# Performance work log

Measured on AMD Instinct MI355X. Metric: run time of the kernel, lower is better.

The kernel has to match this reference:

```python
import jax, jax.numpy as jnp
import numpy as np

SEQ, BATCH, IN_DIM, HID = 2048, 64, 512, 512


def setup_inputs() -> dict:
    key = jax.random.key(0)
    ks = jax.random.split(key, 9)
    cat = IN_DIM + HID
    s = 1.0 / np.sqrt(cat)  # torch Linear default init scale
    inputs = jax.random.normal(ks[0], (SEQ, BATCH, IN_DIM), dtype=jnp.float32)
    def lin(k):
        kw, kb = jax.random.split(k)
        W = jax.random.uniform(kw, (cat, HID), jnp.float32, -s, s)
        b = jax.random.uniform(kb, (HID,), jnp.float32, -s, s)
        return W, b
    Wf, bf = lin(ks[1])
    Wi, bi = lin(ks[2])
    Wg, bg = lin(ks[3])
    Wo, bo = lin(ks[4])
    return {"inputs": inputs, "Wf": Wf, "bf": bf, "Wi": Wi, "bi": bi,
            "Wg": Wg, "bg": bg, "Wo": Wo, "bo": bo}


def reference(inputs, Wf, bf, Wi, bi, Wg, bg, Wo, bo):
    # inputs: (seq, batch, in_dim). Weights stored as (in+hid, hid) so
    # combined @ W + b matches torch's Linear on concat([x, hx]).
    batch = inputs.shape[1]
    hx0 = jnp.zeros((batch, HID), inputs.dtype)
    cx0 = jnp.zeros((batch, HID), inputs.dtype)

    def step(carry, x):
        hx, cx = carry
        combined = jnp.concatenate([x, hx], axis=1)  # (batch, in+hid)
        f = jax.nn.sigmoid(combined @ Wf + bf)
        i = jax.nn.sigmoid(combined @ Wi + bi)
        g = jnp.tanh(combined @ Wg + bg)
        o = jax.nn.sigmoid(combined @ Wo + bo)
        cx = f * cx + i * g
        hx = o * jnp.tanh(cx)
        return (hx, cx), hx

    (hx, cx), outputs = jax.lax.scan(step, (hx0, cx0), inputs)
    return outputs, (hx, cx)
```

## Files before the change

### kernel.cpp

```cpp
#include <hip/hip_runtime.h>
#include <hip/hip_bf16.h>


#define SEQ 2048
#define NBATCH 64
#define IN_DIM 512
#define HID 512
#define NB 64
#define GB 16

typedef __bf16 bf16x8 __attribute__((ext_vector_type(8)));
typedef short s16x8 __attribute__((ext_vector_type(8)));
typedef float f32x4 __attribute__((ext_vector_type(4)));
typedef unsigned int u32;
typedef unsigned short u16;
typedef u32 u32x4 __attribute__((ext_vector_type(4)));

__global__ void lstm_init(u32* ws) {
    __hip_atomic_store(&ws[threadIdx.x], 0u, __ATOMIC_RELAXED,
                       __HIP_MEMORY_SCOPE_AGENT);
}

__device__ inline bf16x8 cvt8(const float* p) {
    f32x4 u = *reinterpret_cast<const f32x4*>(p);
    f32x4 v = *reinterpret_cast<const f32x4*>(p + 4);
    bf16x8 r;
    r[0] = (__bf16)u[0]; r[1] = (__bf16)u[1]; r[2] = (__bf16)u[2]; r[3] = (__bf16)u[3];
    r[4] = (__bf16)v[0]; r[5] = (__bf16)v[1]; r[6] = (__bf16)v[2]; r[7] = (__bf16)v[3];
    return r;
}

__global__ void __launch_bounds__(256, 2) lstm_persistent(
    const float* __restrict__ x,
    const float* __restrict__ Wf, const float* __restrict__ bfp,
    const float* __restrict__ Wi, const float* __restrict__ bip,
    const float* __restrict__ Wg, const float* __restrict__ bgp,
    const float* __restrict__ Wo, const float* __restrict__ bop,
    float* __restrict__ out, u32* __restrict__ flags,
    u32* __restrict__ hbuf )
{
    __shared__ short w_lds[256 * 32];
    __shared__ float red[4 * 2 * 16 * 16];

    const int T    = threadIdx.x;
    const int wave = T >> 6;
    const int lane = T & 63;
    const int quad = lane >> 4;
    const int nl   = lane & 15;

    const int g    = blockIdx.x & 3;
    const int j    = blockIdx.x >> 2;
    const int bg0  = g * GB;
    const int hid0 = j * 8;

    const float* Wp[4] = {Wf, Wi, Wg, Wo};

    bf16x8 bfrag[2][8];
    for (int c = 0; c < 4; ++c) {
        for (int it = 0; it < 4; ++it) {
            int i = it * 256 + T;
            int kl = i >> 2, g4 = i & 3;
            int k = c * 256 + kl;
            bf16x8 v = cvt8(Wp[g4] + (size_t)k * HID + hid0);
            *reinterpret_cast<s16x8*>(&w_lds[kl * 32 + g4 * 8]) =
                __builtin_bit_cast(s16x8, v);
        }
        __syncthreads();
        if (wave == c) {
            #pragma unroll
            for (int nt = 0; nt < 2; ++nt)
                #pragma unroll
                for (int ks = 0; ks < 8; ++ks) {
                    s16x8 tmp;
                    int kbase = ks * 32 + quad * 8;
                    int n = nt * 16 + nl;
                    #pragma unroll
                    for (int kk = 0; kk < 8; ++kk)
                        tmp[kk] = w_lds[(kbase + kk) * 32 + n];
                    bfrag[nt][ks] = __builtin_bit_cast(bf16x8, tmp);
                }
        }
        __syncthreads();
    }

    float bias0 = 0.f, bias1 = 0.f, bias2 = 0.f, bias3 = 0.f, cstate = 0.f;
    if (T < 128) {
        int col = hid0 + (T & 7);
        bias0 = bfp[col]; bias1 = bip[col]; bias2 = bgp[col]; bias3 = bop[col];
    }

    const int aoff = (bg0 + nl) * 512 + (wave & 1) * 256 + quad * 8;
    const u32* myFlags = flags + g * NB;

    for (int t = 0; t < SEQ; ++t) {
        f32x4 acc0 = {0.f, 0.f, 0.f, 0.f};
        f32x4 acc1 = {0.f, 0.f, 0.f, 0.f};

        if (wave < 2) {
            const float* base = x + (size_t)t * (NBATCH * IN_DIM) + aoff;
            #pragma unroll
            for (int ks = 0; ks < 8; ++ks) {
                bf16x8 a = cvt8(base + ks * 32);
                acc0 = __builtin_amdgcn_mfma_f32_16x16x32_bf16(a, bfrag[0][ks], acc0, 0, 0, 0);
                acc1 = __builtin_amdgcn_mfma_f32_16x16x32_bf16(a, bfrag[1][ks], acc1, 0, 0, 0);
            }
        } else if (t > 0) {
            const u32 target = (u32)t;
            const u32* fl = myFlags + lane;
            while (true) {
                u32 f = __hip_atomic_load(fl, __ATOMIC_RELAXED,
                                          __HIP_MEMORY_SCOPE_AGENT);
                if (__all((int)(f >= target))) break;
                __builtin_amdgcn_s_sleep(1);
            }
            asm volatile("" ::: "memory");

            const u32* hb = hbuf
                + (size_t)((t - 1) & 1) * (NBATCH * HID / 2) + (aoff >> 1);
            u32x4 hv[8];
            #pragma unroll
            for (int ks = 0; ks < 8; ++ks) {
                #pragma unroll
                for (int q = 0; q < 4; ++q)
                    hv[ks][q] = __hip_atomic_load(hb + ks * 16 + q,
                                                  __ATOMIC_RELAXED,
                                                  __HIP_MEMORY_SCOPE_AGENT);
            }
            #pragma unroll
            for (int ks = 0; ks < 8; ++ks) {
                bf16x8 a = __builtin_bit_cast(bf16x8, hv[ks]);
                acc0 = __builtin_amdgcn_mfma_f32_16x16x32_bf16(a, bfrag[0][ks], acc0, 0, 0, 0);
                acc1 = __builtin_amdgcn_mfma_f32_16x16x32_bf16(a, bfrag[1][ks], acc1, 0, 0, 0);
            }
        }

        *reinterpret_cast<f32x4*>(&red[((wave * 2 + 0) * 16 + nl) * 16 + quad * 4]) = acc0;
        *reinterpret_cast<f32x4*>(&red[((wave * 2 + 1) * 16 + nl) * 16 + quad * 4]) = acc1;
        __syncthreads();

        if (T < 128) {
            const int m = T >> 3, c8 = T & 7;
            float pre[4];
            #pragma unroll
            for (int q = 0; q < 4; ++q) {
                int n = q * 8 + c8;
                int nt = n >> 4, nn = n & 15;
                float s = 0.f;
                #pragma unroll
                for (int w = 0; w < 4; ++w)
                    s += red[((w * 2 + nt) * 16 + nn) * 16 + m];
                pre[q] = s;
            }
            float fg = 1.f / (1.f + __expf(-(pre[0] + bias0)));
            float ig = 1.f / (1.f + __expf(-(pre[1] + bias1)));
            float gg = 2.f / (1.f + __expf(-2.f * (pre[2] + bias2))) - 1.f;
            float og = 1.f / (1.f + __expf(-(pre[3] + bias3)));
            cstate = fg * cstate + ig * gg;
            float h = og * (2.f / (1.f + __expf(-2.f * cstate)) - 1.f);
            size_t oidx = ((size_t)t * NBATCH + bg0 + m) * HID + hid0 + c8;
            out[oidx] = h;

            u32 mybits = (u32)__builtin_bit_cast(u16, (__bf16)h);
            u32 pbits  = (u32)__shfl_xor((int)mybits, 1, 64);
            if ((T & 1) == 0) {
                u32 packed = mybits | (pbits << 16);
                u32 idx = (u32)((((bg0 + m) * HID) + hid0 + c8) >> 1);
                __hip_atomic_store(hbuf + (size_t)(t & 1) * (NBATCH * HID / 2) + idx,
                                   packed, __ATOMIC_RELAXED,
                                   __HIP_MEMORY_SCOPE_AGENT);
            }
            if (t == SEQ - 1) {
                size_t fin = (size_t)SEQ * NBATCH * HID + (size_t)(bg0 + m) * HID + hid0 + c8;
                out[fin] = h;
                out[fin + NBATCH * HID] = cstate;
            }
        }
        __syncthreads();
        if (T == 0) {
            __hip_atomic_store(const_cast<u32*>(myFlags) + j, (u32)(t + 1),
                               __ATOMIC_RELAXED, __HIP_MEMORY_SCOPE_AGENT);
        }
    }
}

extern "C" void kernel_launch(void* const* d_in, const int* in_sizes, int n_in,
                              void* d_out, int out_size, void* d_ws, size_t ws_size,
                              hipStream_t stream) {
    const float* x  = (const float*)d_in[0];
    const float* Wf = (const float*)d_in[1];
    const float* bf = (const float*)d_in[2];
    const float* Wi = (const float*)d_in[3];
    const float* bi = (const float*)d_in[4];
    const float* Wg = (const float*)d_in[5];
    const float* bg = (const float*)d_in[6];
    const float* Wo = (const float*)d_in[7];
    const float* bo = (const float*)d_in[8];

    u32* flags = (u32*)d_ws;
    u32* hbuf  = (u32*)((char*)d_ws + 4096);

    lstm_init<<<dim3(1), dim3(256), 0, stream>>>(flags);
    lstm_persistent<<<dim3(256), dim3(256), 0, stream>>>(
        x, Wf, bf, Wi, bi, Wg, bg, Wo, bo,
        (float*)d_out, flags, hbuf);
}
```

Before: 10.38 ms.

## Replace step flags with sentinel-valued hidden-state ring buffer polling

```diff
diff --git a/kernel.cpp b/kernel.cpp
--- a/kernel.cpp
+++ b/kernel.cpp
@@ -8,6 +8,8 @@
 #define HID 512
 #define NB 64
 #define GB 16
+#define NSLOT 6
+#define SLOT_U32 (NBATCH * HID / 2)
 
 typedef __bf16 bf16x8 __attribute__((ext_vector_type(8)));
 typedef short s16x8 __attribute__((ext_vector_type(8)));
@@ -16,9 +18,12 @@
 typedef unsigned short u16;
 typedef u32 u32x4 __attribute__((ext_vector_type(4)));
 
-__global__ void lstm_init(u32* ws) {
-    __hip_atomic_store(&ws[threadIdx.x], 0u, __ATOMIC_RELAXED,
-                       __HIP_MEMORY_SCOPE_AGENT);
+__global__ void lstm_init(u32* hbuf) {
+    const u32 n = NSLOT * SLOT_U32;
+    for (u32 i = blockIdx.x * blockDim.x + threadIdx.x; i < n;
+         i += gridDim.x * blockDim.x)
+        __hip_atomic_store(&hbuf[i], 0xFFFFFFFFu, __ATOMIC_RELAXED,
+                           __HIP_MEMORY_SCOPE_AGENT);
 }
 
 __device__ inline bf16x8 cvt8(const float* p) {
@@ -36,11 +41,10 @@
     const float* __restrict__ Wi, const float* __restrict__ bip,
     const float* __restrict__ Wg, const float* __restrict__ bgp,
     const float* __restrict__ Wo, const float* __restrict__ bop,
-    float* __restrict__ out, u32* __restrict__ flags,
-    u32* __restrict__ hbuf )
+    float* __restrict__ out, u32* __restrict__ hbuf)
 {
     __shared__ short w_lds[256 * 32];
-    __shared__ float red[4 * 2 * 16 * 16];
+    __shared__ float red[8 * 16 * 20];
 
     const int T    = threadIdx.x;
     const int wave = T >> 6;
@@ -90,7 +94,10 @@
     }
 
     const int aoff = (bg0 + nl) * 512 + (wave & 1) * 256 + quad * 8;
-    const u32* myFlags = flags + g * NB;
+
+    int slotW = 0;
+    int slotR = 5;
+    int slotP = 3;
 
     for (int t = 0; t < SEQ; ++t) {
         f32x4 acc0 = {0.f, 0.f, 0.f, 0.f};
@@ -105,26 +112,24 @@
                 acc1 = __builtin_amdgcn_mfma_f32_16x16x32_bf16(a, bfrag[1][ks], acc1, 0, 0, 0);
             }
         } else if (t > 0) {
-            const u32 target = (u32)t;
-            const u32* fl = myFlags + lane;
+            const u32* hb = hbuf + (size_t)slotR * SLOT_U32 + (aoff >> 1);
+            u32x4 hv[8];
             while (true) {
-                u32 f = __hip_atomic_load(fl, __ATOMIC_RELAXED,
-                                          __HIP_MEMORY_SCOPE_AGENT);
-                if (__all((int)(f >= target))) break;
+                #pragma unroll
+                for (int ks = 0; ks < 8; ++ks)
+                    #pragma unroll
+                    for (int q = 0; q < 4; ++q)
+                        hv[ks][q] = __hip_atomic_load(hb + ks * 16 + q,
+                                                      __ATOMIC_RELAXED,
+                                                      __HIP_MEMORY_SCOPE_AGENT);
+                u32 bad = 0;
+                #pragma unroll
+                for (int ks = 0; ks < 8; ++ks)
+                    #pragma unroll
+                    for (int q = 0; q < 4; ++q)
+                        bad |= (u32)(hv[ks][q] == 0xFFFFFFFFu);
+                if (__all((int)(bad == 0))) break;
                 __builtin_amdgcn_s_sleep(1);
-            }
-            asm volatile("" ::: "memory");
-
-            const u32* hb = hbuf
-                + (size_t)((t - 1) & 1) * (NBATCH * HID / 2) + (aoff >> 1);
-            u32x4 hv[8];
-            #pragma unroll
-            for (int ks = 0; ks < 8; ++ks) {
-                #pragma unroll
-                for (int q = 0; q < 4; ++q)
-                    hv[ks][q] = __hip_atomic_load(hb + ks * 16 + q,
-                                                  __ATOMIC_RELAXED,
-                                                  __HIP_MEMORY_SCOPE_AGENT);
             }
             #pragma unroll
             for (int ks = 0; ks < 8; ++ks) {
@@ -134,8 +139,8 @@
             }
         }
 
-        *reinterpret_cast<f32x4*>(&red[((wave * 2 + 0) * 16 + nl) * 16 + quad * 4]) = acc0;
-        *reinterpret_cast<f32x4*>(&red[((wave * 2 + 1) * 16 + nl) * 16 + quad * 4]) = acc1;
+        *reinterpret_cast<f32x4*>(&red[((wave * 2 + 0) * 16 + nl) * 20 + quad * 4]) = acc0;
+        *reinterpret_cast<f32x4*>(&red[((wave * 2 + 1) * 16 + nl) * 20 + quad * 4]) = acc1;
         __syncthreads();
 
         if (T < 128) {
@@ -148,7 +153,7 @@
                 float s = 0.f;
                 #pragma unroll
                 for (int w = 0; w < 4; ++w)
-                    s += red[((w * 2 + nt) * 16 + nn) * 16 + m];
+                    s += red[((w * 2 + nt) * 16 + nn) * 20 + m];
                 pre[q] = s;
             }
             float fg = 1.f / (1.f + __expf(-(pre[0] + bias0)));
@@ -165,8 +170,11 @@
             if ((T & 1) == 0) {
                 u32 packed = mybits | (pbits << 16);
                 u32 idx = (u32)((((bg0 + m) * HID) + hid0 + c8) >> 1);
-                __hip_atomic_store(hbuf + (size_t)(t & 1) * (NBATCH * HID / 2) + idx,
+                __hip_atomic_store(hbuf + (size_t)slotW * SLOT_U32 + idx,
                                    packed, __ATOMIC_RELAXED,
+                                   __HIP_MEMORY_SCOPE_AGENT);
+                __hip_atomic_store(hbuf + (size_t)slotP * SLOT_U32 + idx,
+                                   0xFFFFFFFFu, __ATOMIC_RELAXED,
                                    __HIP_MEMORY_SCOPE_AGENT);
             }
             if (t == SEQ - 1) {
@@ -176,10 +184,10 @@
             }
         }
         __syncthreads();
-        if (T == 0) {
-            __hip_atomic_store(const_cast<u32*>(myFlags) + j, (u32)(t + 1),
-                               __ATOMIC_RELAXED, __HIP_MEMORY_SCOPE_AGENT);
-        }
+
+        slotW = (slotW == NSLOT - 1) ? 0 : slotW + 1;
+        slotR = (slotR == NSLOT - 1) ? 0 : slotR + 1;
+        slotP = (slotP == NSLOT - 1) ? 0 : slotP + 1;
     }
 }
 
@@ -196,11 +204,10 @@
     const float* Wo = (const float*)d_in[7];
     const float* bo = (const float*)d_in[8];
 
-    u32* flags = (u32*)d_ws;
-    u32* hbuf  = (u32*)((char*)d_ws + 4096);
-
-    lstm_init<<<dim3(1), dim3(256), 0, stream>>>(flags);
+    u32* hbuf = (u32*)d_ws;
+
+    lstm_init<<<dim3(192), dim3(256), 0, stream>>>(hbuf);
     lstm_persistent<<<dim3(256), dim3(256), 0, stream>>>(
         x, Wf, bf, Wi, bi, Wg, bg, Wo, bo,
-        (float*)d_out, flags, hbuf);
-}
+        (float*)d_out, hbuf);
+}
```

Result: slower. 13.08 ms (+26.0%).
